# Kernel optimization log

Measured on AMD Instinct MI355X. Metric: run time of the kernel, lower is better.

## Reference

```python
import jax, jax.numpy as jnp
import numpy as np

N = 4096
FEAT = 64


def _pairwise_dist(x):
    # x: [N, F] -> symmetric [N, N] Euclidean distance matrix, zero diagonal
    sq = jnp.sum(x * x, axis=-1)
    d2 = sq[:, None] + sq[None, :] - 2.0 * (x @ x.T)
    d = jnp.sqrt(jnp.maximum(d2, 0.0))
    return d * (1.0 - jnp.eye(x.shape[0], dtype=x.dtype))


def setup_inputs() -> dict:
    key = jax.random.key(0)
    k1, k2 = jax.random.split(key)
    x1 = jax.random.normal(k1, (N, FEAT), dtype=jnp.float32)
    x2 = jax.random.normal(k2, (N, FEAT), dtype=jnp.float32)
    return {"d1": _pairwise_dist(x1), "d2": _pairwise_dist(x2)}


def _mst_edges(d):
    # Prim's algorithm, O(N^2). For a distance matrix with generic (distinct)
    # entries the MST is unique and its N-1 edges are exactly the 0-dim
    # persistence pairs returned by the union-find PersistentHomologyCalculation.
    n = d.shape[0]
    INF = jnp.asarray(jnp.finfo(d.dtype).max, d.dtype)
    in_tree = jnp.zeros((n,), dtype=bool).at[0].set(True)
    min_dist = d[0]                       # best edge weight into the tree per node
    parent = jnp.zeros((n,), dtype=jnp.int32)  # tree endpoint of that best edge

    def step(carry, _):
        in_tree, min_dist, parent = carry
        masked = jnp.where(in_tree, INF, min_dist)
        j = jnp.argmin(masked).astype(jnp.int32)
        edge = jnp.stack([parent[j], j])  # (tree node, new node)
        in_tree = in_tree.at[j].set(True)
        dj = d[j]
        upd = (dj < min_dist) & (~in_tree)
        min_dist = jnp.where(upd, dj, min_dist)
        parent = jnp.where(upd, j, parent)
        return (in_tree, min_dist, parent), edge

    _, edges = jax.lax.scan(step, (in_tree, min_dist, parent), None, length=n - 1)
    return edges  # [N-1, 2] int32; d is symmetric so pair order is irrelevant


def reference(d1, d2):
    # Pairings are computed on detached CPU copies in the original -> no grad
    p1 = _mst_edges(jax.lax.stop_gradient(d1))
    p2 = jax.lax.stop_gradient(_mst_edges(jax.lax.stop_gradient(d2)))
    sig1 = d1[p1[:, 0], p1[:, 1]]
    sig2 = d2[p2[:, 0], p2[:, 1]]
    # match_edges == 'symmetric'
    sig1_2 = d2[p1[:, 0], p1[:, 1]]
    sig2_1 = d1[p2[:, 0], p2[:, 1]]
    return jnp.sum((sig1 - sig1_2) ** 2) + jnp.sum((sig2 - sig2_1) ** 2)
```

## Files before the change

### kernel.cpp

```cpp
#include <hip/hip_runtime.h>
#include <stdint.h>


#define N        4096
#define NROUNDS  12

typedef unsigned long long u64;
typedef uint32_t u32;

#define INFK (~0ull)

struct Ws {
    u64 best[2][N];
    u32 comp[2][N];
    u32 edges[2][N];
    u32 ncomp[2];
    u32 pad[14];
    u64 bm[2][N * 64];
};

__device__ __forceinline__ u64 umin64(u64 a, u64 b) { return a < b ? a : b; }

__device__ __forceinline__ u64 shfl_xor_u64(u64 x, int off) {
    u32 lo = (u32)x, hi = (u32)(x >> 32);
    lo = (u32)__shfl_xor((int)lo, off, 64);
    hi = (u32)__shfl_xor((int)hi, off, 64);
    return ((u64)hi << 32) | lo;
}

__launch_bounds__(256, 8)
__global__ void scanA_k(const float* __restrict__ d1, const float* __restrict__ d2,
                        Ws* __restrict__ ws) {
    const int m = blockIdx.x >> 10;
    const int wave = threadIdx.x >> 6, lane = threadIdx.x & 63;
    const int v = ((blockIdx.x & 1023) << 2) + wave;
    const float4* __restrict__ row4 = (const float4*)((m ? d2 : d1) + (size_t)v * N);

    const u32 uv = (u32)v;
    u64 bmin = INFK;
    #pragma unroll
    for (int j = 0; j < 16; ++j) {
        const int c = lane + 64 * j;
        float4 w = row4[c];
        const u32 c0 = (u32)(4 * c);
        if (c0 + 0 != uv) bmin = umin64(bmin, (((u64)__float_as_uint(w.x)) << 12) | (c0 + 0));
        if (c0 + 1 != uv) bmin = umin64(bmin, (((u64)__float_as_uint(w.y)) << 12) | (c0 + 1));
        if (c0 + 2 != uv) bmin = umin64(bmin, (((u64)__float_as_uint(w.z)) << 12) | (c0 + 2));
        if (c0 + 3 != uv) bmin = umin64(bmin, (((u64)__float_as_uint(w.w)) << 12) | (c0 + 3));
    }
    ws->bm[m][(size_t)v * 64 + lane] = bmin;

    u64 rowmin = bmin;
    #pragma unroll
    for (int off = 1; off <= 32; off <<= 1)
        rowmin = umin64(rowmin, shfl_xor_u64(rowmin, off));

    if (lane == 0) {
        u32 u  = (u32)rowmin & 0xFFFu;
        u64 wb = rowmin >> 12;
        u32 lo = min(uv, u), hi = max(uv, u);
        ws->best[m][v]  = (wb << 24) | ((u64)lo << 12) | (u64)hi;
        ws->comp[m][v]  = uv;
        ws->edges[m][v] = (uv << 12) | uv;
    }
    if (threadIdx.x == 0 && (blockIdx.x & 1023) == 0)
        ws->ncomp[m] = (u32)N;
}

__launch_bounds__(256, 8)
__global__ void scan2_k(const float* __restrict__ d1, const float* __restrict__ d2,
                        Ws* __restrict__ ws) {
    const int m = blockIdx.x >> 10;
    if (ws->ncomp[m] <= 1u) return;
    const int wave = threadIdx.x >> 6, lane = threadIdx.x & 63;
    const int v = ((blockIdx.x & 1023) << 2) + wave;

    const float* __restrict__ dm = m ? d2 : d1;
    const u32*   __restrict__ cm = ws->comp[m];
    u64* __restrict__ bmrow = ws->bm[m] + (size_t)v * 64;

    const u32 cv = cm[v];
    u64 key = bmrow[lane];
    bool cross = false;
    if (key != INFK) cross = (cm[(u32)key & 0xFFFu] != cv);

    u64 kb = cross ? key : INFK;
    #pragma unroll
    for (int off = 1; off <= 32; off <<= 1)
        kb = umin64(kb, shfl_xor_u64(kb, off));

    const bool need = (!cross) && (key < kb);
    u64 nm = INFK;
    if (need) {
        const float4* __restrict__ row4 = (const float4*)(dm + (size_t)v * N);
        const uint4*  __restrict__ c4   = (const uint4*)cm;
        #pragma unroll
        for (int j = 0; j < 16; ++j) {
            const int c = lane + 64 * j;
            float4 w = row4[c];
            uint4 cu = c4[c];
            u32 c0 = (u32)(4 * c);
            if (cu.x != cv) nm = umin64(nm, (((u64)__float_as_uint(w.x)) << 12) | (c0 + 0));
            if (cu.y != cv) nm = umin64(nm, (((u64)__float_as_uint(w.y)) << 12) | (c0 + 1));
            if (cu.z != cv) nm = umin64(nm, (((u64)__float_as_uint(w.z)) << 12) | (c0 + 2));
            if (cu.w != cv) nm = umin64(nm, (((u64)__float_as_uint(w.w)) << 12) | (c0 + 3));
        }
        bmrow[lane] = nm;
    }
    u64 kb2 = need ? nm : INFK;
    #pragma unroll
    for (int off = 1; off <= 32; off <<= 1)
        kb2 = umin64(kb2, shfl_xor_u64(kb2, off));

    u64 fin = umin64(kb, kb2);
    if (lane == 0 && fin != INFK) {
        u32 u  = (u32)fin & 0xFFFu;
        u64 wb = fin >> 12;
        u32 lo = min((u32)v, u), hi = max((u32)v, u);
        u64 g  = (wb << 24) | ((u64)lo << 12) | (u64)hi;
        if (g < ws->best[m][cv])
            atomicMin(&ws->best[m][cv], g);
    }
}

__launch_bounds__(256, 8)
__global__ void scanF_k(const float* __restrict__ d1, const float* __restrict__ d2,
                        Ws* __restrict__ ws, int first) {
    const int m = blockIdx.x >> 10;
    if (!first && ws->ncomp[m] <= 1u) return;
    const int wave = threadIdx.x >> 6, lane = threadIdx.x & 63;
    const int v = ((blockIdx.x & 1023) << 2) + wave;
    const float* __restrict__ dm = m ? d2 : d1;
    const u32*   __restrict__ cm = ws->comp[m];
    const float4* __restrict__ row4 = (const float4*)(dm + (size_t)v * N);
    const uint4*  __restrict__ c4   = (const uint4*)cm;
    const u32 cv = first ? (u32)v : cm[v];
    u64 kmin = INFK;
    #pragma unroll
    for (int j = 0; j < 16; ++j) {
        const int c = lane + 64 * j;
        float4 w = row4[c];
        uint4 cu;
        if (!first) cu = c4[c];
        const u32 c0 = (u32)(4 * c);
        bool x0, x1, x2, x3;
        if (first) {
            x0 = (c0+0 != cv); x1 = (c0+1 != cv); x2 = (c0+2 != cv); x3 = (c0+3 != cv);
        } else {
            x0 = (cu.x != cv); x1 = (cu.y != cv); x2 = (cu.z != cv); x3 = (cu.w != cv);
        }
        if (x0) kmin = umin64(kmin, (((u64)__float_as_uint(w.x)) << 12) | (c0 + 0));
        if (x1) kmin = umin64(kmin, (((u64)__float_as_uint(w.y)) << 12) | (c0 + 1));
        if (x2) kmin = umin64(kmin, (((u64)__float_as_uint(w.z)) << 12) | (c0 + 2));
        if (x3) kmin = umin64(kmin, (((u64)__float_as_uint(w.w)) << 12) | (c0 + 3));
    }
    #pragma unroll
    for (int off = 1; off <= 32; off <<= 1)
        kmin = umin64(kmin, shfl_xor_u64(kmin, off));
    if (lane == 0 && kmin != INFK) {
        u32 u  = (u32)kmin & 0xFFFu;
        u64 wb = kmin >> 12;
        u32 lo = min((u32)v, u), hi = max((u32)v, u);
        u64 g  = (wb << 24) | ((u64)lo << 12) | (u64)hi;
        if (first) {
            ws->best[m][v]  = g;
            ws->comp[m][v]  = (u32)v;
            ws->edges[m][v] = ((u32)v << 12) | (u32)v;
        } else if (g < ws->best[m][cv]) {
            atomicMin(&ws->best[m][cv], g);
        }
    }
    if (first && threadIdx.x == 0 && (blockIdx.x & 1023) == 0)
        ws->ncomp[m] = (u32)N;
}

__launch_bounds__(1024, 1)
__global__ void hook_k(const float* __restrict__ d1, const float* __restrict__ d2,
                       Ws* __restrict__ ws, float* __restrict__ out, int fin) {
    const int m = blockIdx.x;
    const int tid = threadIdx.x;
    const int lane = tid & 63, wave = tid >> 6;

    __shared__ u32 compL[N];
    __shared__ u32 nxtA[N];
    __shared__ u32 nxtB[N];
    __shared__ u32 red[16];
    __shared__ float fpart[16];

    if (ws->ncomp[m] > 1u) {
        u32* __restrict__ gcomp = ws->comp[m];
        u64* __restrict__ best  = ws->best[m];

        {
            uint4* dst = (uint4*)compL;
            const uint4* src = (const uint4*)gcomp;
            if (tid < N / 4) dst[tid] = src[tid];
        }
        __syncthreads();

        bool isroot[4];
        u64  bkey[4];

        #pragma unroll
        for (int k = 0; k < 4; ++k) {
            int i = tid + k * 1024;
            u32 x = (u32)i;
            bool r = (compL[i] == (u32)i);
            isroot[k] = r;
            u64 g = 0;
            if (r) {
                g = best[i];
                u32 lo = (u32)(g >> 12) & 0xFFFu;
                u32 hi = (u32)g & 0xFFFu;
                u32 cl = compL[lo], ch = compL[hi];
                x = (cl == (u32)i) ? ch : cl;
            }
            bkey[k] = g;
            nxtA[i] = x;
        }
        __syncthreads();

        #pragma unroll
        for (int k = 0; k < 4; ++k) {
            int i = tid + k * 1024;
            u32 nn = (u32)i;
            if (isroot[k]) {
                u32 o = nxtA[i];
                bool mutual = (nxtA[o] == (u32)i);
                nn = (mutual && ((u32)i < o)) ? (u32)i : o;
                if (nn != (u32)i)
                    ws->edges[m][i] = (u32)(bkey[k] & 0xFFFFFFu);
            }
            nxtB[i] = nn;
        }
        __syncthreads();

        for (int s = 0; s < 12; ++s) {
            u32 changed = 0;
            #pragma unroll
            for (int k = 0; k < 4; ++k) {
                int i = tid + k * 1024;
                u32 a = nxtB[i];
                u32 t = nxtB[a];
                if (t != a) changed = 1u;
                nxtB[i] = t;
            }
            if (!__syncthreads_or((int)changed)) break;
        }

        u32 cnt = 0;
        #pragma unroll
        for (int k = 0; k < 4; ++k) {
            int i = tid + k * 1024;
            if (isroot[k] && nxtB[i] == (u32)i) cnt++;
        }
        #pragma unroll
        for (int off = 32; off >= 1; off >>= 1) cnt += (u32)__shfl_down((int)cnt, off, 64);
        if (lane == 0) red[wave] = cnt;
        __syncthreads();

        #pragma unroll
        for (int k = 0; k < 4; ++k) {
            int i = tid + k * 1024;
            gcomp[i] = nxtB[compL[i]];
            if (isroot[k]) best[i] = INFK;
        }
        if (tid == 0) {
            u32 t = 0;
            #pragma unroll
            for (int w = 0; w < 16; ++w) t += red[w];
            ws->ncomp[m] = t;
        }
    }

    if (fin) {
        __syncthreads();
        float acc = 0.f;
        #pragma unroll
        for (int k = 0; k < 4; ++k) {
            int i = tid + k * 1024;
            u32 pk = ws->edges[m][i];
            u32 lo = (pk >> 12) & 0xFFFu, hi = pk & 0xFFFu;
            size_t off = (size_t)lo * N + hi;
            float df = d1[off] - d2[off];
            acc += df * df;
        }
        #pragma unroll
        for (int off = 32; off >= 1; off >>= 1) acc += __shfl_down(acc, off, 64);
        if (lane == 0) fpart[wave] = acc;
        __syncthreads();
        if (tid == 0) {
            float t = 0.f;
            #pragma unroll
            for (int w = 0; w < 16; ++w) t += fpart[w];
            atomicAdd(out, t);
        }
    }
}

extern "C" void kernel_launch(void* const* d_in, const int* in_sizes, int n_in,
                              void* d_out, int out_size, void* d_ws, size_t ws_size,
                              hipStream_t stream) {
    (void)in_sizes; (void)n_in; (void)out_size;
    const float* d1 = (const float*)d_in[0];
    const float* d2 = (const float*)d_in[1];
    float* out = (float*)d_out;
    Ws* ws = (Ws*)d_ws;
    const bool big = (ws_size >= sizeof(Ws));

    hipMemsetAsync(d_out, 0, sizeof(float), stream);
    for (int r = 0; r < NROUNDS; ++r) {
        if (big) {
            if (r == 0) scanA_k<<<dim3(2048), dim3(256), 0, stream>>>(d1, d2, ws);
            else        scan2_k<<<dim3(2048), dim3(256), 0, stream>>>(d1, d2, ws);
        } else {
            scanF_k<<<dim3(2048), dim3(256), 0, stream>>>(d1, d2, ws, r == 0 ? 1 : 0);
        }
        hook_k<<<dim3(2), dim3(1024), 0, stream>>>(d1, d2, ws, out, r == NROUNDS - 1 ? 1 : 0);
    }
}
```

Measured before the change: 267.2 us.

## Store per-lane bucket minima over contiguous column chunks for strided rescans

The initial row scan now computes, for each lane, the minimum over a contiguous 64-column chunk using intra-16-lane shuffles, rather than a lane-strided set of columns. The rescan kernel switches to matching contiguous per-lane chunk reads and uses four independent min accumulators. Contiguous buckets make each bucket a tighter column range, so they can be reused more selectively. The cost is extra shuffles in scanA and uncoalesced, per-lane-strided loads in the rescan path.

```diff
diff --git a/kernel.cpp b/kernel.cpp
--- a/kernel.cpp
+++ b/kernel.cpp
@@ -37,20 +37,27 @@
     const float4* __restrict__ row4 = (const float4*)((m ? d2 : d1) + (size_t)v * N);
 
     const u32 uv = (u32)v;
-    u64 bmin = INFK;
+    u64 rowacc = INFK;
+    u64 kept   = INFK;
     #pragma unroll
     for (int j = 0; j < 16; ++j) {
         const int c = lane + 64 * j;
         float4 w = row4[c];
         const u32 c0 = (u32)(4 * c);
-        if (c0 + 0 != uv) bmin = umin64(bmin, (((u64)__float_as_uint(w.x)) << 12) | (c0 + 0));
-        if (c0 + 1 != uv) bmin = umin64(bmin, (((u64)__float_as_uint(w.y)) << 12) | (c0 + 1));
-        if (c0 + 2 != uv) bmin = umin64(bmin, (((u64)__float_as_uint(w.z)) << 12) | (c0 + 2));
-        if (c0 + 3 != uv) bmin = umin64(bmin, (((u64)__float_as_uint(w.w)) << 12) | (c0 + 3));
-    }
-    ws->bm[m][(size_t)v * 64 + lane] = bmin;
-
-    u64 rowmin = bmin;
+        u64 k0 = (c0 + 0 != uv) ? ((((u64)__float_as_uint(w.x)) << 12) | (c0 + 0)) : INFK;
+        u64 k1 = (c0 + 1 != uv) ? ((((u64)__float_as_uint(w.y)) << 12) | (c0 + 1)) : INFK;
+        u64 k2 = (c0 + 2 != uv) ? ((((u64)__float_as_uint(w.z)) << 12) | (c0 + 2)) : INFK;
+        u64 k3 = (c0 + 3 != uv) ? ((((u64)__float_as_uint(w.w)) << 12) | (c0 + 3)) : INFK;
+        u64 lm = umin64(umin64(k0, k1), umin64(k2, k3));
+        rowacc = umin64(rowacc, lm);
+        #pragma unroll
+        for (int off = 1; off <= 8; off <<= 1)
+            lm = umin64(lm, shfl_xor_u64(lm, off));
+        if ((lane & 15) == j) kept = lm;
+    }
+    ws->bm[m][(size_t)v * 64 + (4 * (lane & 15) + (lane >> 4))] = kept;
+
+    u64 rowmin = rowacc;
     #pragma unroll
     for (int off = 1; off <= 32; off <<= 1)
         rowmin = umin64(rowmin, shfl_xor_u64(rowmin, off));
@@ -94,17 +101,19 @@
     if (need) {
         const float4* __restrict__ row4 = (const float4*)(dm + (size_t)v * N);
         const uint4*  __restrict__ c4   = (const uint4*)cm;
+        const int base = lane * 16;
+        u64 n0 = INFK, n1 = INFK, n2 = INFK, n3 = INFK;
         #pragma unroll
         for (int j = 0; j < 16; ++j) {
-            const int c = lane + 64 * j;
-            float4 w = row4[c];
-            uint4 cu = c4[c];
-            u32 c0 = (u32)(4 * c);
-            if (cu.x != cv) nm = umin64(nm, (((u64)__float_as_uint(w.x)) << 12) | (c0 + 0));
-            if (cu.y != cv) nm = umin64(nm, (((u64)__float_as_uint(w.y)) << 12) | (c0 + 1));
-            if (cu.z != cv) nm = umin64(nm, (((u64)__float_as_uint(w.z)) << 12) | (c0 + 2));
-            if (cu.w != cv) nm = umin64(nm, (((u64)__float_as_uint(w.w)) << 12) | (c0 + 3));
-        }
+            float4 w  = row4[base + j];
+            uint4  cu = c4[base + j];
+            const u32 c0 = (u32)(4 * (base + j));
+            if (cu.x != cv) n0 = umin64(n0, (((u64)__float_as_uint(w.x)) << 12) | (c0 + 0));
+            if (cu.y != cv) n1 = umin64(n1, (((u64)__float_as_uint(w.y)) << 12) | (c0 + 1));
+            if (cu.z != cv) n2 = umin64(n2, (((u64)__float_as_uint(w.z)) << 12) | (c0 + 2));
+            if (cu.w != cv) n3 = umin64(n3, (((u64)__float_as_uint(w.w)) << 12) | (c0 + 3));
+        }
+        nm = umin64(umin64(n0, n1), umin64(n2, n3));
         bmrow[lane] = nm;
     }
     u64 kb2 = need ? nm : INFK;
```

New measurement: 413.2 us. 54.6% more time.
